# Kernel optimization log

Hardware: AMD Instinct MI355X
Metric: run time of the kernel (lower is better)

The kernel has to match this reference:

```python
import jax, jax.numpy as jnp
import numpy as np

N, F_IN, H, C, E = 100000, 128, 64, 40, 1600000
NEG_SLOPE = 0.2


def setup_inputs() -> dict:
    key = jax.random.key(0)
    ks = jax.random.split(key, 12)
    s = 0.1
    return {
        "x": jax.random.normal(ks[0], (N, F_IN), jnp.float32),
        "edge_index": jax.random.randint(ks[1], (2, E), 0, N, jnp.int32),
        "W1": jax.random.normal(ks[2], (F_IN, H), jnp.float32) * s,
        "a_src1": jax.random.normal(ks[3], (H,), jnp.float32) * s,
        "a_dst1": jax.random.normal(ks[4], (H,), jnp.float32) * s,
        "b1": jnp.zeros((H,), jnp.float32),
        "W2": jax.random.normal(ks[5], (H, H), jnp.float32) * s,
        "a_src2": jax.random.normal(ks[6], (H,), jnp.float32) * s,
        "a_dst2": jax.random.normal(ks[7], (H,), jnp.float32) * s,
        "b2": jnp.zeros((H,), jnp.float32),
        "Wl": jax.random.normal(ks[8], (H, C), jnp.float32) * s,
        "bl": jnp.zeros((C,), jnp.float32),
    }


def gat_conv(x, src, dst, W, a_src, a_dst, b):
    # PyG GATConv, heads=1, self-loops already appended to (src, dst)
    h = x @ W                                   # [N, H]
    alpha_s = h @ a_src                         # [N]
    alpha_d = h @ a_dst                         # [N]
    e = jax.nn.leaky_relu(alpha_s[src] + alpha_d[dst], NEG_SLOPE)  # [E]
    # segment softmax over incoming edges of each target node
    m = jax.ops.segment_max(e, dst, num_segments=x.shape[0])
    ex = jnp.exp(e - m[dst])
    denom = jax.ops.segment_sum(ex, dst, num_segments=x.shape[0])
    w = ex / (denom[dst] + 1e-16)               # [E]
    out = jax.ops.segment_sum(h[src] * w[:, None], dst, num_segments=x.shape[0])
    return out + b


def reference(x, edge_index, W1, a_src1, a_dst1, b1, W2, a_src2, a_dst2, b2, Wl, bl):
    n = x.shape[0]
    loops = jnp.arange(n, dtype=edge_index.dtype)
    src = jnp.concatenate([edge_index[0], loops])
    dst = jnp.concatenate([edge_index[1], loops])
    h = gat_conv(x, src, dst, W1, a_src1, a_dst1, b1)
    h = jax.nn.relu(h)  # dropout p=0 -> identity
    h = gat_conv(h, src, dst, W2, a_src2, a_dst2, b2)
    logits = h @ Wl + bl
    return jax.nn.log_softmax(logits, axis=-1)
```

## Files before the change

### kernel.cpp

```cpp
#include <hip/hip_runtime.h>
#include <math.h>


#define NEG_SLOPE 0.2f
#define NEG_BIG -3.0e38f

#define BSHIFT 9
#define BSIZE 512
#define BCAP 12288
#define EPB 4096

typedef __bf16 bf16x8 __attribute__((ext_vector_type(8)));
typedef __bf16 bf16x4 __attribute__((ext_vector_type(4)));
typedef float f32x4 __attribute__((ext_vector_type(4)));

__device__ __forceinline__ float lrelu(float x) {
    return x >= 0.f ? x : NEG_SLOPE * x;
}


__global__ __launch_bounds__(256) void bucket_scatter(const int* __restrict__ src,
                                                      const int* __restrict__ dst,
                                                      int* __restrict__ bucketCount,
                                                      unsigned* __restrict__ ebuf,
                                                      int E) {
    __shared__ int hist[256], base[256], cur[256];
    const int t = threadIdx.x;
    hist[t] = 0;
    __syncthreads();
    const int e0 = blockIdx.x * EPB;
    const int e1 = min(e0 + EPB, E);
    for (int e = e0 + t; e < e1; e += 256)
        atomicAdd(&hist[dst[e] >> BSHIFT], 1);
    __syncthreads();
    if (hist[t] > 0) base[t] = atomicAdd(&bucketCount[t], hist[t]);
    cur[t] = 0;
    __syncthreads();
    for (int e = e0 + t; e < e1; e += 256) {
        int d = dst[e];
        int b = d >> BSHIFT;
        int r = atomicAdd(&cur[b], 1);
        ebuf[(size_t)b * BCAP + base[b] + r] =
            ((unsigned)src[e] << BSHIFT) | (unsigned)(d & (BSIZE - 1));
    }
}

__global__ __launch_bounds__(256) void bucket_scan(const int* __restrict__ bucketCount,
                                                   int* __restrict__ bucketBase,
                                                   int* __restrict__ offs,
                                                   int N, int E, int nbuck) {
    __shared__ int sh[256];
    const int t = threadIdx.x;
    int v = (t < nbuck) ? bucketCount[t] : 0;
    sh[t] = v;
    __syncthreads();
    for (int d = 1; d < 256; d <<= 1) {
        int x = (t >= d) ? sh[t - d] : 0;
        __syncthreads();
        sh[t] += x;
        __syncthreads();
    }
    bucketBase[t] = sh[t] - v;
    if (t == 0) offs[N] = E;
}

__global__ __launch_bounds__(512) void bucket_csr(const unsigned* __restrict__ ebuf,
                                                  const int* __restrict__ bucketCount,
                                                  const int* __restrict__ bucketBase,
                                                  int* __restrict__ offs,
                                                  int* __restrict__ csr, int N) {
    __shared__ int hist[512], scan[512];
    const int b = blockIdx.x;
    const int t = threadIdx.x;
    const int cnt = bucketCount[b];
    const int gbase = bucketBase[b];
    const unsigned* __restrict__ eb = ebuf + (size_t)b * BCAP;
    hist[t] = 0;
    __syncthreads();
    for (int i = t; i < cnt; i += 512)
        atomicAdd(&hist[eb[i] & (BSIZE - 1)], 1);
    __syncthreads();
    int v = hist[t];
    scan[t] = v;
    __syncthreads();
    for (int d = 1; d < 512; d <<= 1) {
        int x = (t >= d) ? scan[t - d] : 0;
        __syncthreads();
        scan[t] += x;
        __syncthreads();
    }
    int excl = scan[t] - v;
    int n = b * BSIZE + t;
    if (n < N) offs[n] = gbase + excl;
    hist[t] = excl;
    __syncthreads();
    for (int i = t; i < cnt; i += 512) {
        unsigned rec = eb[i];
        int pos = atomicAdd(&hist[rec & (BSIZE - 1)], 1);
        csr[gbase + pos] = (int)(rec >> BSHIFT);
    }
}


template <int K>
__global__ __launch_bounds__(256) void gemm_mfma(const float* __restrict__ X,
                                                 const float* __restrict__ W,
                                                 const float* __restrict__ a_src,
                                                 const float* __restrict__ a_dst,
                                                 __bf16* __restrict__ Hout,
                                                 float* __restrict__ as_,
                                                 float* __restrict__ ad_,
                                                 int N, int nTiles) {
    __shared__ __bf16 Whi[64][K + 8];
    __shared__ __bf16 Wlo[64][K + 8];
    for (int idx = threadIdx.x; idx < K * 64; idx += 256) {
        int k = idx >> 6, n = idx & 63;
        float w = W[idx];
        __bf16 hi = (__bf16)w;
        Whi[n][k] = hi;
        Wlo[n][k] = (__bf16)(w - (float)hi);
    }
    __syncthreads();

    const int lane  = threadIdx.x & 63;
    const int wave  = threadIdx.x >> 6;
    const int row16 = lane & 15;
    const int quad  = lane >> 4;

    float asv[4], adv[4];
#pragma unroll
    for (int t = 0; t < 4; ++t) {
        asv[t] = a_src[t * 16 + row16];
        adv[t] = a_dst[t * 16 + row16];
    }

    for (int tile = blockIdx.x; tile < nTiles; tile += gridDim.x) {
        const int nbase = tile * 64;
        int gn = nbase + wave * 16 + row16;
        if (gn >= N) gn = N - 1;
        const float* __restrict__ xp = X + (size_t)gn * K + quad * 8;

        float4 xv[K / 16];
#pragma unroll
        for (int c = 0; c < K / 32; ++c) {
            xv[2 * c]     = *(const float4*)(xp + c * 32);
            xv[2 * c + 1] = *(const float4*)(xp + c * 32 + 4);
        }

        f32x4 acc[4] = {{0.f, 0.f, 0.f, 0.f}, {0.f, 0.f, 0.f, 0.f},
                        {0.f, 0.f, 0.f, 0.f}, {0.f, 0.f, 0.f, 0.f}};
#pragma unroll
        for (int kc = 0; kc < K; kc += 32) {
            float xs[8];
            *(float4*)&xs[0] = xv[kc / 16];
            *(float4*)&xs[4] = xv[kc / 16 + 1];
            bf16x8 ahi, alo;
#pragma unroll
            for (int j = 0; j < 8; ++j) {
                __bf16 hi = (__bf16)xs[j];
                ahi[j] = hi;
                alo[j] = (__bf16)(xs[j] - (float)hi);
            }
#pragma unroll
            for (int t = 0; t < 4; ++t) {
                bf16x8 bhi = *(const bf16x8*)&Whi[t * 16 + row16][kc + quad * 8];
                bf16x8 blo = *(const bf16x8*)&Wlo[t * 16 + row16][kc + quad * 8];
                acc[t] = __builtin_amdgcn_mfma_f32_16x16x32_bf16(ahi, bhi, acc[t], 0, 0, 0);
                acc[t] = __builtin_amdgcn_mfma_f32_16x16x32_bf16(ahi, blo, acc[t], 0, 0, 0);
                acc[t] = __builtin_amdgcn_mfma_f32_16x16x32_bf16(alo, bhi, acc[t], 0, 0, 0);
            }
        }

        float ps[4] = {0.f, 0.f, 0.f, 0.f};
        float pd[4] = {0.f, 0.f, 0.f, 0.f};
#pragma unroll
        for (int t = 0; t < 4; ++t) {
#pragma unroll
            for (int r = 0; r < 4; ++r) {
                int gm = nbase + wave * 16 + quad * 4 + r;
                if (gm < N) Hout[(size_t)gm * 64 + t * 16 + row16] = (__bf16)acc[t][r];
                ps[r] = fmaf(acc[t][r], asv[t], ps[r]);
                pd[r] = fmaf(acc[t][r], adv[t], pd[r]);
            }
        }
#pragma unroll
        for (int r = 0; r < 4; ++r) {
#pragma unroll
            for (int d = 1; d < 16; d <<= 1) {
                ps[r] += __shfl_xor(ps[r], d, 64);
                pd[r] += __shfl_xor(pd[r], d, 64);
            }
        }
        if (row16 == 0) {
#pragma unroll
            for (int r = 0; r < 4; ++r) {
                int gm = nbase + wave * 16 + quad * 4 + r;
                if (gm < N) { as_[gm] = ps[r]; ad_[gm] = pd[r]; }
            }
        }
    }
}


__global__ __launch_bounds__(256) void gat_agg(const __bf16* __restrict__ h,
                                               const float* __restrict__ as_,
                                               const float* __restrict__ ad_,
                                               const float* __restrict__ bias,
                                               const int* __restrict__ offs,
                                               const int* __restrict__ csr,
                                               float* __restrict__ out,
                                               int N, int do_relu) {
    int gtid = blockIdx.x * blockDim.x + threadIdx.x;
    int n = __builtin_amdgcn_readfirstlane(gtid >> 6);
    if (n >= N) return;
    const int lane = threadIdx.x & 63;
    const int g  = lane >> 4;
    const int fl = lane & 15;

    int beg = offs[n], end = offs[n + 1];
    float adn = ad_[n];
    float p_self = __expf(lrelu(as_[n] + adn));

    float den = p_self;
    float ax, ay, az, aw;
    {
        bf16x4 t = *(const bf16x4*)(h + (size_t)n * 64 + fl * 4);
        float m0 = (g == 0) ? p_self : 0.f;
        ax = m0 * (float)t[0];
        ay = m0 * (float)t[1];
        az = m0 * (float)t[2];
        aw = m0 * (float)t[3];
    }

    for (int c0 = beg; c0 < end; c0 += 64) {
        int cnt = end - c0;
        if (cnt > 64) cnt = 64;
        int   s_l = (lane < cnt) ? csr[c0 + lane] : 0;
        float p_l = (lane < cnt) ? __expf(lrelu(as_[s_l] + adn)) : 0.f;
        float csum = p_l;
#pragma unroll
        for (int d = 32; d; d >>= 1) csum += __shfl_xor(csum, d, 64);
        den += csum;

        int rounds = (cnt + 3) >> 2;
        for (int r = 0; r < rounds; r += 4) {
            int j0 = (r + 0) * 4 + g, j1 = (r + 1) * 4 + g;
            int j2 = (r + 2) * 4 + g, j3 = (r + 3) * 4 + g;
            float w0 = __shfl(p_l, j0, 64), w1 = __shfl(p_l, j1, 64);
            float w2 = __shfl(p_l, j2, 64), w3 = __shfl(p_l, j3, 64);
            int s0 = __shfl(s_l, j0, 64), s1 = __shfl(s_l, j1, 64);
            int s2 = __shfl(s_l, j2, 64), s3 = __shfl(s_l, j3, 64);
            bf16x4 h0 = *(const bf16x4*)(h + (size_t)s0 * 64 + fl * 4);
            bf16x4 h1 = *(const bf16x4*)(h + (size_t)s1 * 64 + fl * 4);
            bf16x4 h2 = *(const bf16x4*)(h + (size_t)s2 * 64 + fl * 4);
            bf16x4 h3 = *(const bf16x4*)(h + (size_t)s3 * 64 + fl * 4);
            ax = fmaf(w0, (float)h0[0], ax); ay = fmaf(w0, (float)h0[1], ay);
            az = fmaf(w0, (float)h0[2], az); aw = fmaf(w0, (float)h0[3], aw);
            ax = fmaf(w1, (float)h1[0], ax); ay = fmaf(w1, (float)h1[1], ay);
            az = fmaf(w1, (float)h1[2], az); aw = fmaf(w1, (float)h1[3], aw);
            ax = fmaf(w2, (float)h2[0], ax); ay = fmaf(w2, (float)h2[1], ay);
            az = fmaf(w2, (float)h2[2], az); aw = fmaf(w2, (float)h2[3], aw);
            ax = fmaf(w3, (float)h3[0], ax); ay = fmaf(w3, (float)h3[1], ay);
            az = fmaf(w3, (float)h3[2], az); aw = fmaf(w3, (float)h3[3], aw);
        }
    }

#pragma unroll
    for (int d = 16; d <= 32; d <<= 1) {
        ax += __shfl_xor(ax, d, 64);
        ay += __shfl_xor(ay, d, 64);
        az += __shfl_xor(az, d, 64);
        aw += __shfl_xor(aw, d, 64);
    }
    if (g == 0) {
        float inv = 1.f / (den + 1e-16f);
        const float4 b4 = *(const float4*)(bias + fl * 4);
        float4 o;
        o.x = fmaf(ax, inv, b4.x);
        o.y = fmaf(ay, inv, b4.y);
        o.z = fmaf(az, inv, b4.z);
        o.w = fmaf(aw, inv, b4.w);
        if (do_relu) {
            o.x = fmaxf(o.x, 0.f); o.y = fmaxf(o.y, 0.f);
            o.z = fmaxf(o.z, 0.f); o.w = fmaxf(o.w, 0.f);
        }
        *(float4*)(out + (size_t)n * 64 + fl * 4) = o;
    }
}


__global__ __launch_bounds__(256) void final_lsm(const float* __restrict__ h,
                                                 const float* __restrict__ Wl,
                                                 const float* __restrict__ bl,
                                                 float* __restrict__ out,
                                                 int N, int nTiles) {
    __shared__ __bf16 Whi[48][72];
    __shared__ __bf16 Wlo[48][72];
    __shared__ float bls[48];
    for (int idx = threadIdx.x; idx < 48 * 64; idx += 256) {
        int c = idx >> 6, k = idx & 63;
        float w = (c < 40) ? Wl[k * 40 + c] : 0.f;
        __bf16 hi = (__bf16)w;
        Whi[c][k] = hi;
        Wlo[c][k] = (__bf16)(w - (float)hi);
    }
    if (threadIdx.x < 48) bls[threadIdx.x] = (threadIdx.x < 40) ? bl[threadIdx.x] : 0.f;
    __syncthreads();

    const int lane  = threadIdx.x & 63;
    const int wave  = threadIdx.x >> 6;
    const int col16 = lane & 15;
    const int quad  = lane >> 4;

    for (int tile = blockIdx.x; tile < nTiles; tile += gridDim.x) {
        const int nbase = tile * 64;
        int gn = nbase + wave * 16 + col16;
        if (gn >= N) gn = N - 1;
        const float* __restrict__ xp = h + (size_t)gn * 64 + quad * 8;
        float4 xv[4];
        xv[0] = *(const float4*)(xp);
        xv[1] = *(const float4*)(xp + 4);
        xv[2] = *(const float4*)(xp + 32);
        xv[3] = *(const float4*)(xp + 36);

        f32x4 acc[3] = {{0.f, 0.f, 0.f, 0.f}, {0.f, 0.f, 0.f, 0.f},
                        {0.f, 0.f, 0.f, 0.f}};
#pragma unroll
        for (int kc = 0; kc < 64; kc += 32) {
            float xs[8];
            *(float4*)&xs[0] = xv[kc / 16];
            *(float4*)&xs[4] = xv[kc / 16 + 1];
            bf16x8 ahi, alo;
#pragma unroll
            for (int j = 0; j < 8; ++j) {
                __bf16 hi = (__bf16)xs[j];
                ahi[j] = hi;
                alo[j] = (__bf16)(xs[j] - (float)hi);
            }
#pragma unroll
            for (int t = 0; t < 3; ++t) {
                bf16x8 bhi = *(const bf16x8*)&Whi[t * 16 + col16][kc + quad * 8];
                bf16x8 blo = *(const bf16x8*)&Wlo[t * 16 + col16][kc + quad * 8];
                acc[t] = __builtin_amdgcn_mfma_f32_16x16x32_bf16(ahi, bhi, acc[t], 0, 0, 0);
                acc[t] = __builtin_amdgcn_mfma_f32_16x16x32_bf16(ahi, blo, acc[t], 0, 0, 0);
                acc[t] = __builtin_amdgcn_mfma_f32_16x16x32_bf16(alo, bhi, acc[t], 0, 0, 0);
            }
        }

#pragma unroll
        for (int r = 0; r < 4; ++r) {
            int gm = nbase + wave * 16 + quad * 4 + r;
            float l0 = acc[0][r] + bls[col16];
            float l1 = acc[1][r] + bls[16 + col16];
            float l2 = (col16 < 8) ? (acc[2][r] + bls[32 + col16]) : NEG_BIG;
            float mx = fmaxf(fmaxf(l0, l1), l2);
#pragma unroll
            for (int d = 1; d < 16; d <<= 1) mx = fmaxf(mx, __shfl_xor(mx, d, 64));
            float s = __expf(l0 - mx) + __expf(l1 - mx) +
                      ((col16 < 8) ? __expf(l2 - mx) : 0.f);
#pragma unroll
            for (int d = 1; d < 16; d <<= 1) s += __shfl_xor(s, d, 64);
            float lse = mx + __logf(s);
            if (gm < N) {
                out[(size_t)gm * 40 + col16]      = l0 - lse;
                out[(size_t)gm * 40 + 16 + col16] = l1 - lse;
                if (col16 < 8) out[(size_t)gm * 40 + 32 + col16] = l2 - lse;
            }
        }
    }
}


extern "C" void kernel_launch(void* const* d_in, const int* in_sizes, int n_in,
                              void* d_out, int out_size, void* d_ws, size_t ws_size,
                              hipStream_t stream) {
    const float* x      = (const float*)d_in[0];
    const int*   ei     = (const int*)d_in[1];
    const float* W1     = (const float*)d_in[2];
    const float* a_src1 = (const float*)d_in[3];
    const float* a_dst1 = (const float*)d_in[4];
    const float* b1     = (const float*)d_in[5];
    const float* W2     = (const float*)d_in[6];
    const float* a_src2 = (const float*)d_in[7];
    const float* a_dst2 = (const float*)d_in[8];
    const float* b2     = (const float*)d_in[9];
    const float* Wl     = (const float*)d_in[10];
    const float* bl     = (const float*)d_in[11];

    const int N = in_sizes[0] / 128;
    const int E = in_sizes[1] / 2;
    const int* src = ei;
    const int* dst = ei + E;
    const int nbuck = (N + BSIZE - 1) >> BSHIFT;

    char* p = (char*)d_ws;
    auto alloc = [&](size_t bytes) -> void* {
        void* r = (void*)p;
        p += (bytes + 255) & ~(size_t)255;
        return r;
    };
    int*      offs        = (int*)alloc((size_t)(N + 1) * 4);
    int*      bucketCount = (int*)alloc(256 * 4);
    int*      bucketBase  = (int*)alloc(256 * 4);
    unsigned* ebuf        = (unsigned*)alloc((size_t)nbuck * BCAP * 4);
    int*      csr         = (int*)alloc((size_t)E * 4);
    __bf16*   hbf         = (__bf16*)alloc((size_t)N * 64 * 2);
    float*    bufB        = (float*)alloc((size_t)N * 64 * 4);
    float*    as_         = (float*)alloc((size_t)N * 4);
    float*    ad_         = (float*)alloc((size_t)N * 4);

    hipMemsetAsync(bucketCount, 0, 256 * 4, stream);

    bucket_scatter<<<(E + EPB - 1) / EPB, 256, 0, stream>>>(src, dst, bucketCount, ebuf, E);
    bucket_scan<<<1, 256, 0, stream>>>(bucketCount, bucketBase, offs, N, E, nbuck);
    bucket_csr<<<nbuck, 512, 0, stream>>>(ebuf, bucketCount, bucketBase, offs, csr, N);

    const int nTiles = (N + 63) / 64;
    int aggBlocks = (N * 64 + 255) / 256;

    gemm_mfma<128><<<1024, 256, 0, stream>>>(x, W1, a_src1, a_dst1, hbf, as_, ad_, N, nTiles);
    gat_agg<<<aggBlocks, 256, 0, stream>>>(hbf, as_, ad_, b1, offs, csr, bufB, N, 1);
    gemm_mfma<64><<<1024, 256, 0, stream>>>(bufB, W2, a_src2, a_dst2, hbf, as_, ad_, N, nTiles);
    gat_agg<<<aggBlocks, 256, 0, stream>>>(hbf, as_, ad_, b2, offs, csr, bufB, N, 0);
    final_lsm<<<nTiles, 256, 0, stream>>>(bufB, Wl, bl, (float*)d_out, N, nTiles);
}
```

Baseline: 296.2 us.

## Fuse edge bucket scatter with first-layer GEMM and fold bucket scan into CSR

The edge bucket-scatter pass and the first-layer MFMA GEMM now run as two independent block ranges of a single launch, so the memory-bound scatter and the compute-bound GEMM share the GPU at the same time. The separate single-block bucket scan kernel is removed, and every bucket_csr block now recomputes the 256-entry prefix sum over bucket counts itself. This saves two launches and lets the two preprocessing tasks overlap. In exchange, the scatter blocks reserve the GEMM's larger shared memory allocation, which can lower their occupancy, and the bucket scan work is repeated in every CSR block.

Result: faster. 284.8 us (-3.8%).

```diff
diff --git a/kernel.cpp b/kernel.cpp
--- a/kernel.cpp
+++ b/kernel.cpp
@@ -19,61 +19,150 @@
 }
 
 
-__global__ __launch_bounds__(256) void bucket_scatter(const int* __restrict__ src,
-                                                      const int* __restrict__ dst,
-                                                      int* __restrict__ bucketCount,
-                                                      unsigned* __restrict__ ebuf,
-                                                      int E) {
+__global__ __launch_bounds__(256) void fused_scatter_gemm(
+        const int* __restrict__ src, const int* __restrict__ dst,
+        int* __restrict__ bucketCount, unsigned* __restrict__ ebuf, int E, int SB,
+        const float* __restrict__ X, const float* __restrict__ W,
+        const float* __restrict__ a_src, const float* __restrict__ a_dst,
+        __bf16* __restrict__ Hout, float* __restrict__ as_, float* __restrict__ ad_,
+        int N, int nTiles) {
+    constexpr int K = 128;
+    __shared__ __bf16 Whi[64][K + 8];
+    __shared__ __bf16 Wlo[64][K + 8];
     __shared__ int hist[256], base[256], cur[256];
-    const int t = threadIdx.x;
-    hist[t] = 0;
-    __syncthreads();
-    const int e0 = blockIdx.x * EPB;
-    const int e1 = min(e0 + EPB, E);
-    for (int e = e0 + t; e < e1; e += 256)
-        atomicAdd(&hist[dst[e] >> BSHIFT], 1);
-    __syncthreads();
-    if (hist[t] > 0) base[t] = atomicAdd(&bucketCount[t], hist[t]);
-    cur[t] = 0;
-    __syncthreads();
-    for (int e = e0 + t; e < e1; e += 256) {
-        int d = dst[e];
-        int b = d >> BSHIFT;
-        int r = atomicAdd(&cur[b], 1);
-        ebuf[(size_t)b * BCAP + base[b] + r] =
-            ((unsigned)src[e] << BSHIFT) | (unsigned)(d & (BSIZE - 1));
-    }
-}
-
-__global__ __launch_bounds__(256) void bucket_scan(const int* __restrict__ bucketCount,
-                                                   int* __restrict__ bucketBase,
-                                                   int* __restrict__ offs,
-                                                   int N, int E, int nbuck) {
-    __shared__ int sh[256];
-    const int t = threadIdx.x;
-    int v = (t < nbuck) ? bucketCount[t] : 0;
-    sh[t] = v;
-    __syncthreads();
-    for (int d = 1; d < 256; d <<= 1) {
-        int x = (t >= d) ? sh[t - d] : 0;
-        __syncthreads();
-        sh[t] += x;
-        __syncthreads();
-    }
-    bucketBase[t] = sh[t] - v;
-    if (t == 0) offs[N] = E;
-}
+
+    if (blockIdx.x < (unsigned)SB) {
+        const int t = threadIdx.x;
+        hist[t] = 0;
+        __syncthreads();
+        const int e0 = blockIdx.x * EPB;
+        const int e1 = min(e0 + EPB, E);
+        for (int e = e0 + t; e < e1; e += 256)
+            atomicAdd(&hist[dst[e] >> BSHIFT], 1);
+        __syncthreads();
+        if (hist[t] > 0) base[t] = atomicAdd(&bucketCount[t], hist[t]);
+        cur[t] = 0;
+        __syncthreads();
+        for (int e = e0 + t; e < e1; e += 256) {
+            int d = dst[e];
+            int b = d >> BSHIFT;
+            int r = atomicAdd(&cur[b], 1);
+            ebuf[(size_t)b * BCAP + base[b] + r] =
+                ((unsigned)src[e] << BSHIFT) | (unsigned)(d & (BSIZE - 1));
+        }
+        return;
+    }
+
+    const int gbid = blockIdx.x - SB;
+    for (int idx = threadIdx.x; idx < K * 64; idx += 256) {
+        int k = idx >> 6, n = idx & 63;
+        float w = W[idx];
+        __bf16 hi = (__bf16)w;
+        Whi[n][k] = hi;
+        Wlo[n][k] = (__bf16)(w - (float)hi);
+    }
+    __syncthreads();
+
+    const int lane  = threadIdx.x & 63;
+    const int wave  = threadIdx.x >> 6;
+    const int row16 = lane & 15;
+    const int quad  = lane >> 4;
+
+    float asv[4], adv[4];
+#pragma unroll
+    for (int t = 0; t < 4; ++t) {
+        asv[t] = a_src[t * 16 + row16];
+        adv[t] = a_dst[t * 16 + row16];
+    }
+
+    for (int tile = gbid; tile < nTiles; tile += 1024) {
+        const int nbase = tile * 64;
+        int gn = nbase + wave * 16 + row16;
+        if (gn >= N) gn = N - 1;
+        const float* __restrict__ xp = X + (size_t)gn * K + quad * 8;
+
+        float4 xv[K / 16];
+#pragma unroll
+        for (int c = 0; c < K / 32; ++c) {
+            xv[2 * c]     = *(const float4*)(xp + c * 32);
+            xv[2 * c + 1] = *(const float4*)(xp + c * 32 + 4);
+        }
+
+        f32x4 acc[4] = {{0.f, 0.f, 0.f, 0.f}, {0.f, 0.f, 0.f, 0.f},
+                        {0.f, 0.f, 0.f, 0.f}, {0.f, 0.f, 0.f, 0.f}};
+#pragma unroll
+        for (int kc = 0; kc < K; kc += 32) {
+            float xs[8];
+            *(float4*)&xs[0] = xv[kc / 16];
+            *(float4*)&xs[4] = xv[kc / 16 + 1];
+            bf16x8 ahi, alo;
+#pragma unroll
+            for (int j = 0; j < 8; ++j) {
+                __bf16 hi = (__bf16)xs[j];
+                ahi[j] = hi;
+                alo[j] = (__bf16)(xs[j] - (float)hi);
+            }
+#pragma unroll
+            for (int t = 0; t < 4; ++t) {
+                bf16x8 bhi = *(const bf16x8*)&Whi[t * 16 + row16][kc + quad * 8];
+                bf16x8 blo = *(const bf16x8*)&Wlo[t * 16 + row16][kc + quad * 8];
+                acc[t] = __builtin_amdgcn_mfma_f32_16x16x32_bf16(ahi, bhi, acc[t], 0, 0, 0);
+                acc[t] = __builtin_amdgcn_mfma_f32_16x16x32_bf16(ahi, blo, acc[t], 0, 0, 0);
+                acc[t] = __builtin_amdgcn_mfma_f32_16x16x32_bf16(alo, bhi, acc[t], 0, 0, 0);
+            }
+        }
+
+        float ps[4] = {0.f, 0.f, 0.f, 0.f};
+        float pd[4] = {0.f, 0.f, 0.f, 0.f};
+#pragma unroll
+        for (int t = 0; t < 4; ++t) {
+#pragma unroll
+            for (int r = 0; r < 4; ++r) {
+                int gm = nbase + wave * 16 + quad * 4 + r;
+                if (gm < N) Hout[(size_t)gm * 64 + t * 16 + row16] = (__bf16)acc[t][r];
+                ps[r] = fmaf(acc[t][r], asv[t], ps[r]);
+                pd[r] = fmaf(acc[t][r], adv[t], pd[r]);
+            }
+        }
+#pragma unroll
+        for (int r = 0; r < 4; ++r) {
+#pragma unroll
+            for (int d = 1; d < 16; d <<= 1) {
+                ps[r] += __shfl_xor(ps[r], d, 64);
+                pd[r] += __shfl_xor(pd[r], d, 64);
+            }
+        }
+        if (row16 == 0) {
+#pragma unroll
+            for (int r = 0; r < 4; ++r) {
+                int gm = nbase + wave * 16 + quad * 4 + r;
+                if (gm < N) { as_[gm] = ps[r]; ad_[gm] = pd[r]; }
+            }
+        }
+    }
+}
+
 
 __global__ __launch_bounds__(512) void bucket_csr(const unsigned* __restrict__ ebuf,
                                                   const int* __restrict__ bucketCount,
-                                                  const int* __restrict__ bucketBase,
                                                   int* __restrict__ offs,
-                                                  int* __restrict__ csr, int N) {
-    __shared__ int hist[512], scan[512];
+                                                  int* __restrict__ csr, int N, int E) {
+    __shared__ int hist[512], scan[512], bscan[256];
     const int b = blockIdx.x;
     const int t = threadIdx.x;
+
+    if (t < 256) bscan[t] = bucketCount[t];
+    __syncthreads();
+    for (int d = 1; d < 256; d <<= 1) {
+        int x = (t < 256 && t >= d) ? bscan[t - d] : 0;
+        __syncthreads();
+        if (t < 256) bscan[t] += x;
+        __syncthreads();
+    }
     const int cnt = bucketCount[b];
-    const int gbase = bucketBase[b];
+    const int gbase = bscan[b] - cnt;
+    if (b == 0 && t == 0) offs[N] = E;
+
     const unsigned* __restrict__ eb = ebuf + (size_t)b * BCAP;
     hist[t] = 0;
     __syncthreads();
@@ -392,6 +481,7 @@
     const int* src = ei;
     const int* dst = ei + E;
     const int nbuck = (N + BSIZE - 1) >> BSHIFT;
+    const int SB = (E + EPB - 1) / EPB;
 
     char* p = (char*)d_ws;
     auto alloc = [&](size_t bytes) -> void* {
@@ -401,7 +491,6 @@
     };
     int*      offs        = (int*)alloc((size_t)(N + 1) * 4);
     int*      bucketCount = (int*)alloc(256 * 4);
-    int*      bucketBase  = (int*)alloc(256 * 4);
     unsigned* ebuf        = (unsigned*)alloc((size_t)nbuck * BCAP * 4);
     int*      csr         = (int*)alloc((size_t)E * 4);
     __bf16*   hbf         = (__bf16*)alloc((size_t)N * 64 * 2);
@@ -411,14 +500,13 @@
 
     hipMemsetAsync(bucketCount, 0, 256 * 4, stream);
 
-    bucket_scatter<<<(E + EPB - 1) / EPB, 256, 0, stream>>>(src, dst, bucketCount, ebuf, E);
-    bucket_scan<<<1, 256, 0, stream>>>(bucketCount, bucketBase, offs, N, E, nbuck);
-    bucket_csr<<<nbuck, 512, 0, stream>>>(ebuf, bucketCount, bucketBase, offs, csr, N);
-
     const int nTiles = (N + 63) / 64;
     int aggBlocks = (N * 64 + 255) / 256;
 
-    gemm_mfma<128><<<1024, 256, 0, stream>>>(x, W1, a_src1, a_dst1, hbf, as_, ad_, N, nTiles);
+    fused_scatter_gemm<<<SB + 1024, 256, 0, stream>>>(
+        src, dst, bucketCount, ebuf, E, SB,
+        x, W1, a_src1, a_dst1, hbf, as_, ad_, N, nTiles);
+    bucket_csr<<<nbuck, 512, 0, stream>>>(ebuf, bucketCount, offs, csr, N, E);
     gat_agg<<<aggBlocks, 256, 0, stream>>>(hbf, as_, ad_, b1, offs, csr, bufB, N, 1);
     gemm_mfma<64><<<1024, 256, 0, stream>>>(bufB, W2, a_src2, a_dst2, hbf, as_, ad_, N, nTiles);
     gat_agg<<<aggBlocks, 256, 0, stream>>>(hbf, as_, ad_, b2, offs, csr, bufB, N, 0);
```
